# Kernel optimization log

Hardware: AMD Instinct MI355X
Metric: run time of the kernel (lower is better)

Reference implementation:

```python
import jax, jax.numpy as jnp
import numpy as np

D_IN, D_H, BATCH = 4096, 512, 8192


def _layernorm(x, g, b, eps=1e-5):
    mu = jnp.mean(x, axis=-1, keepdims=True)
    var = jnp.var(x, axis=-1, keepdims=True)
    return (x - mu) * jax.lax.rsqrt(var + eps) * g + b


def setup_inputs() -> dict:
    key = jax.random.key(0)
    ks = jax.random.split(key, 10)
    x = jax.random.normal(ks[0], (BATCH, D_IN), jnp.float32)
    h = jax.random.normal(ks[1], (BATCH, D_H), jnp.float32)
    s1 = 1.0 / np.sqrt(D_IN + D_H)
    W1 = jax.random.uniform(ks[2], (D_IN + D_H, D_H), jnp.float32, -s1, s1)
    b1 = jnp.zeros((D_H,), jnp.float32)
    ln1_g = jnp.ones((D_H,), jnp.float32)
    ln1_b = jnp.zeros((D_H,), jnp.float32)
    s2 = 1.0 / np.sqrt(D_H)
    W2 = jax.random.uniform(ks[3], (D_H, 3 * D_H), jnp.float32, -s2, s2)
    b2 = jnp.zeros((3 * D_H,), jnp.float32)
    base_tau = jnp.ones((D_H,), jnp.float32)  # time_constant_init = 1.0
    base_A = jax.random.normal(ks[4], (D_H, D_H), jnp.float32) * 0.1
    idx = jnp.arange(D_H)
    base_A = base_A.at[idx, idx].set(-0.5)
    base_B = jax.random.normal(ks[5], (D_IN, D_H), jnp.float32) * 0.1
    hn_g = jnp.ones((D_H,), jnp.float32)
    hn_b = jnp.zeros((D_H,), jnp.float32)
    return {"x": x, "h": h, "W1": W1, "b1": b1, "ln1_g": ln1_g, "ln1_b": ln1_b,
            "W2": W2, "b2": b2, "base_tau": base_tau, "base_A": base_A,
            "base_B": base_B, "hn_g": hn_g, "hn_b": hn_b}


def reference(x, h, W1, b1, ln1_g, ln1_b, W2, b2, base_tau, base_A, base_B, hn_g, hn_b):
    dt = 0.1
    # time_net hypernetwork
    xh = jnp.concatenate([x, h], axis=-1)                 # [B, D_IN+D_H]
    t = _layernorm(xh @ W1 + b1, ln1_g, ln1_b)
    t = jax.nn.gelu(t, approximate=False)
    params = t @ W2 + b2                                  # [B, 3*D_H]
    tau_s, A_s, B_s = jnp.split(params, 3, axis=-1)
    tau = base_tau * (jax.nn.sigmoid(tau_s) * 2.0)        # [B, D_H]
    A_row = 1.0 + 0.5 * jnp.tanh(A_s)                     # per-sample row scale of A
    B_col = 1.0 + 0.5 * jnp.tanh(B_s)                     # per-sample col scale of B
    # A[b] = base_A * A_row[b][:,None]; h @ A[b].T == (h @ base_A.T) * A_row[b]
    recurrent = (h @ base_A.T) * A_row                    # [B, D_H]
    # B[b] = base_B * B_col[b][None,:]; x @ B[b] == (x @ base_B) * B_col[b]
    input_term = (x @ base_B) * B_col                     # [B, D_H]
    dhdt = -h / (tau + 1e-8) + jnp.tanh(recurrent + input_term)
    new_h = _layernorm(h + dt * dhdt, hn_g, hn_b)
    return new_h
```

## Files before the change

kernel.cpp:

```cpp
#include <hip/hip_runtime.h>

#define BATCH 8192
#define DIN 4096
#define DH 512

typedef float f32x4 __attribute__((ext_vector_type(4)));
typedef float f32x2 __attribute__((ext_vector_type(2)));
typedef short s16x8 __attribute__((ext_vector_type(8)));
typedef unsigned short u16x2 __attribute__((ext_vector_type(2)));
typedef unsigned short u16x4 __attribute__((ext_vector_type(4)));
typedef unsigned short u16x8 __attribute__((ext_vector_type(8)));

static __device__ __forceinline__ unsigned short f2bf(float f) {
  unsigned int u = __float_as_uint(f);
  u += 0x7FFFu + ((u >> 16) & 1u);
  return (unsigned short)(u >> 16);
}
static __device__ __forceinline__ float bf2f(unsigned short s) {
  return __uint_as_float(((unsigned int)s) << 16);
}

typedef const __attribute__((address_space(1))) unsigned int* gas_ptr;
typedef __attribute__((address_space(3))) unsigned int* las_ptr;
static __device__ __forceinline__ void gl_lds16(const unsigned short* g, unsigned short* l) {
  __builtin_amdgcn_global_load_lds((gas_ptr)g, (las_ptr)l, 16, 0, 0);
}

static __device__ __forceinline__ void transpose_body(
    const float* __restrict__ in, int C,
    unsigned short* __restrict__ out, int ldo, int row_off,
    int bx, int by, float (*tl)[33])
{
  const int tid = threadIdx.x;
  const int tx = tid & 31, ty = tid >> 5;
  const int c0 = bx * 32, r0 = by * 32;
#pragma unroll
  for (int i = 0; i < 4; i++)
    tl[ty + 8 * i][tx] = in[(size_t)(r0 + ty + 8 * i) * C + c0 + tx];
  __syncthreads();
#pragma unroll
  for (int i = 0; i < 4; i++)
    out[(size_t)(row_off + c0 + ty + 8 * i) * ldo + r0 + tx] = f2bf(tl[tx][ty + 8 * i]);
}

__global__ __launch_bounds__(256) void prep_all_k(
    const float* __restrict__ x, unsigned short* __restrict__ xbf,
    const float* __restrict__ h, unsigned short* __restrict__ hbf,
    const float* __restrict__ base_A, unsigned short* __restrict__ Abf,
    const float* __restrict__ W1, const float* __restrict__ base_B,
    unsigned short* __restrict__ BTcat,
    const float* __restrict__ W2, unsigned short* __restrict__ W2T)
{
  __shared__ float tl[32][33];
  const int b = blockIdx.x;
  const int tid = threadIdx.x;
  const int KC = DIN + DH;
  if (b < 32768) {
    const int i = (b * 256 + tid) * 4;
    f32x4 v = *(const f32x4*)(x + i);
    u16x4 p = { f2bf(v[0]), f2bf(v[1]), f2bf(v[2]), f2bf(v[3]) };
    *(u16x4*)(xbf + i) = p;
  } else if (b < 36864) {
    const int i = ((b - 32768) * 256 + tid) * 4;
    f32x4 v = *(const f32x4*)(h + i);
    u16x4 p = { f2bf(v[0]), f2bf(v[1]), f2bf(v[2]), f2bf(v[3]) };
    *(u16x4*)(hbf + i) = p;
  } else if (b < 37120) {
    const int i = ((b - 36864) * 256 + tid) * 4;
    f32x4 v = *(const f32x4*)(base_A + i);
    u16x4 p = { f2bf(v[0]), f2bf(v[1]), f2bf(v[2]), f2bf(v[3]) };
    *(u16x4*)(Abf + i) = p;
  } else if (b < 39424) {
    const int bb = b - 37120;
    transpose_body(W1, DH, BTcat, KC, 0, bb & 15, bb >> 4, tl);
  } else if (b < 41472) {
    const int bb = b - 39424;
    transpose_body(base_B, DH, BTcat, KC, DH, bb & 15, bb >> 4, tl);
  } else if (b < 41600) {
    const int gid = (b - 41472) * 256 + tid;
    const int row = gid >> 6, c = (gid & 63) * 8;
    u16x8 z = { 0, 0, 0, 0, 0, 0, 0, 0 };
    *(u16x8*)(BTcat + (size_t)(DH + row) * KC + DIN + c) = z;
  } else {
    const int bb = b - 41600;
    transpose_body(W2, 3 * DH, W2T, DH, 0, bb % 48, bb / 48, tl);
  }
}

template<int EPI>
static __device__ __forceinline__ void gemm2_engine(
    const unsigned short* __restrict__ A0, int lda0, int K0,
    const unsigned short* __restrict__ A1, int lda1,
    const unsigned short* __restrict__ BT, int ldb,
    unsigned short* __restrict__ C0, int ldc,
    unsigned short* __restrict__ C1,
    const float* __restrict__ bias,
    const float* __restrict__ base_tau,
    int mb, int nb, int K, char* smem)
{
  unsigned short* As = (unsigned short*)smem;
  unsigned short* Bs = (unsigned short*)(smem + 32768);
  float* red = (float*)smem;

  const int tid = threadIdx.x;
  const int lane = tid & 63;
  const int wid = tid >> 6;
  const int grp = wid >> 2;
  const int wg  = wid & 3;
  const int wm = (wg >> 1) * 64;
  const int wn = (wg & 1) * 64;
  const int srow = lane >> 2;
  const int scol = ((lane & 3) ^ ((lane >> 3) & 3)) * 8;
  const int fr = lane & 15;
  const int fk = ((lane >> 4) ^ ((lane >> 1) & 3)) * 8;
  const int NT2 = K / 64;

  f32x4 acc[4][4];
#pragma unroll
  for (int i = 0; i < 4; i++)
#pragma unroll
    for (int j = 0; j < 4; j++)
      acc[i][j] = (f32x4){ 0.f, 0.f, 0.f, 0.f };

  auto STAGE = [&](int buf, int per) {
    const int tk = 2 * per + grp;
    const int k0 = tk * 32;
    const bool s0 = (k0 < K0);
    const unsigned short* Ab = s0 ? A0 : A1;
    const int ld = s0 ? lda0 : lda1;
    const int ko = (s0 ? k0 : k0 - K0) + scol;
    unsigned short* ab = As + (grp * 2 + buf) * 4096 + (32 * wg) * 32;
    unsigned short* bb = Bs + (grp * 2 + buf) * 4096 + (32 * wg) * 32;
#pragma unroll
    for (int c = 0; c < 2; c++) {
      const int r = 32 * wg + c * 16 + srow;
      gl_lds16(Ab + (size_t)(mb + r) * ld + ko, ab + c * 16 * 32);
      gl_lds16(BT + (size_t)(nb + r) * ldb + k0 + scol, bb + c * 16 * 32);
    }
  };

  STAGE(0, 0);
  asm volatile("s_waitcnt vmcnt(0)" ::: "memory");
  __builtin_amdgcn_s_barrier();

  int buf = 0;
  for (int t = 0; t < NT2; t++) {
    if (t + 1 < NT2) STAGE(buf ^ 1, t + 1);

    const unsigned short* ar = As + (grp * 2 + buf) * 4096;
    const unsigned short* br = Bs + (grp * 2 + buf) * 4096;
    s16x8 af[4], bv[4];
#pragma unroll
    for (int mi = 0; mi < 4; mi++)
      af[mi] = *(const s16x8*)(ar + (wm + mi * 16 + fr) * 32 + fk);
#pragma unroll
    for (int ni = 0; ni < 4; ni++)
      bv[ni] = *(const s16x8*)(br + (wn + ni * 16 + fr) * 32 + fk);

    asm volatile("s_waitcnt lgkmcnt(0)" ::: "memory");
    __builtin_amdgcn_sched_barrier(0);

#pragma unroll
    for (int mi = 0; mi < 4; mi++)
#pragma unroll
      for (int ni = 0; ni < 4; ni++)
        acc[mi][ni] = __builtin_amdgcn_mfma_f32_16x16x32_bf16(
            af[mi], bv[ni], acc[mi][ni], 0, 0, 0);

    asm volatile("s_waitcnt vmcnt(0)" ::: "memory");
    __builtin_amdgcn_s_barrier();
    buf ^= 1;
  }

  if (grp == 1) {
#pragma unroll
    for (int mi = 0; mi < 4; mi++)
#pragma unroll
      for (int ni = 0; ni < 4; ni++)
        *(f32x4*)(red + (((wg * 4 + mi) * 4 + ni) * 64 + lane) * 4) = acc[mi][ni];
  }
  __syncthreads();
  if (grp != 0) return;

  const int rb = (lane >> 4) * 4;
#pragma unroll
  for (int mi = 0; mi < 4; mi++) {
#pragma unroll
    for (int ni = 0; ni < 4; ni++) {
      f32x4 o = *(const f32x4*)(red + (((wg * 4 + mi) * 4 + ni) * 64 + lane) * 4);
      acc[mi][ni] += o;
#pragma unroll
      for (int r = 0; r < 4; r++) {
        const int row = mb + wm + mi * 16 + rb + r;
        const int col = nb + wn + ni * 16 + fr;
        float v = acc[mi][ni][r];
        if (EPI == 3) {
          if (col < DH) C0[(size_t)row * DH + col] = f2bf(v + bias[col]);
          else          C1[(size_t)row * DH + (col - DH)] = f2bf(v);
        } else if (EPI == 2) {
          C0[(size_t)row * ldc + col] = f2bf(v);
        } else if (EPI == 1) {
          v += bias[col];
          if ((col >> 9) == 0) {
            const float s = 1.0f / (1.0f + expf(-v));
            v = 1.0f / (base_tau[col & (DH - 1)] * 2.0f * s + 1e-8f);
          } else {
            v = 1.0f + 0.5f * tanhf(v);
          }
          C0[(size_t)row * ldc + col] = f2bf(v);
        }
      }
    }
  }
}

__global__ __launch_bounds__(512, 4) void fused_gemm_k(
    const unsigned short* __restrict__ xbf,
    const unsigned short* __restrict__ hbf,
    const unsigned short* __restrict__ BTcat,
    unsigned short* __restrict__ pre1,
    unsigned short* __restrict__ rawB,
    const float* __restrict__ b1)
{
  __shared__ __align__(16) char smem[65536];
  const int cpx = gridDim.x >> 3;
  const int virt = (blockIdx.x & 7) * cpx + (blockIdx.x >> 3);
  const int mb = (virt & 63) * 128;
  const int nb = (virt >> 6) * 128;
  gemm2_engine<3>(xbf, DIN, DIN, hbf, DH, BTcat, DIN + DH,
                  pre1, DH, rawB, b1, nullptr, mb, nb, DIN + DH, smem);
}

__global__ __launch_bounds__(512, 4) void tail_gemm_k(
    const unsigned short* __restrict__ hbf,
    const unsigned short* __restrict__ Abf,
    const unsigned short* __restrict__ tbf,
    const unsigned short* __restrict__ W2T,
    unsigned short* __restrict__ rawA,
    unsigned short* __restrict__ scales,
    const float* __restrict__ b2,
    const float* __restrict__ base_tau)
{
  __shared__ __align__(16) char smem[65536];
  const int b = blockIdx.x;
  if (b < 768) {
    const int mb = (b & 63) * 128, nb = (b >> 6) * 128;
    gemm2_engine<1>(tbf, DH, DH, nullptr, 0, W2T, DH,
                    scales, 3 * DH, nullptr, b2, base_tau, mb, nb, DH, smem);
  } else {
    const int b2i = b - 768;
    const int mb = (b2i & 63) * 128, nb = (b2i >> 6) * 128;
    gemm2_engine<2>(hbf, DH, DH, nullptr, 0, Abf, DH,
                    rawA, DH, nullptr, nullptr, nullptr, mb, nb, DH, smem);
  }
}

__device__ __forceinline__ float block_sum256(float v, float* red) {
#pragma unroll
  for (int m = 32; m >= 1; m >>= 1) v += __shfl_xor(v, m, 64);
  __syncthreads();
  if ((threadIdx.x & 63) == 0) red[threadIdx.x >> 6] = v;
  __syncthreads();
  return red[0] + red[1] + red[2] + red[3];
}

__global__ __launch_bounds__(256) void ln_gelu_k(
    const unsigned short* __restrict__ pre,
    const float* __restrict__ g, const float* __restrict__ b,
    unsigned short* __restrict__ t)
{
  __shared__ float red[4];
  const int row = blockIdx.x;
  const int c = threadIdx.x * 2;
  const size_t ro = (size_t)row * DH;
  u16x2 raw = *(const u16x2*)(pre + ro + c);
  const float v0 = bf2f(raw[0]), v1 = bf2f(raw[1]);
  const float mu = block_sum256(v0 + v1, red) * (1.0f / DH);
  const float d0 = v0 - mu, d1 = v1 - mu;
  const float var = block_sum256(d0 * d0 + d1 * d1, red) * (1.0f / DH);
  const float inv = rsqrtf(var + 1e-5f);
  const float y0 = d0 * inv * g[c] + b[c];
  const float y1 = d1 * inv * g[c + 1] + b[c + 1];
  u16x2 o = { f2bf(0.5f * y0 * (1.0f + erff(y0 * 0.70710678118f))),
              f2bf(0.5f * y1 * (1.0f + erff(y1 * 0.70710678118f))) };
  *(u16x2*)(t + ro + c) = o;
}

__global__ __launch_bounds__(256) void final_k(
    const float* __restrict__ h,
    const unsigned short* __restrict__ rawA,
    const unsigned short* __restrict__ rawB,
    const unsigned short* __restrict__ scales,
    const float* __restrict__ hn_g, const float* __restrict__ hn_b,
    float* __restrict__ out)
{
  __shared__ float red[4];
  const int row = blockIdx.x;
  const int c = threadIdx.x * 2;
  const size_t ro = (size_t)row * DH;
  f32x2 hv = *(const f32x2*)(h + ro + c);
  u16x2 ra = *(const u16x2*)(rawA + ro + c);
  u16x2 rb = *(const u16x2*)(rawB + ro + c);
  const unsigned short* sc = scales + (size_t)row * (3 * DH);
  u16x2 ti  = *(const u16x2*)(sc + c);
  u16x2 arw = *(const u16x2*)(sc + DH + c);
  u16x2 bcl = *(const u16x2*)(sc + 2 * DH + c);
  const float u0 = hv[0] + 0.1f * (-hv[0] * bf2f(ti[0])
                 + tanhf(bf2f(ra[0]) * bf2f(arw[0]) + bf2f(rb[0]) * bf2f(bcl[0])));
  const float u1 = hv[1] + 0.1f * (-hv[1] * bf2f(ti[1])
                 + tanhf(bf2f(ra[1]) * bf2f(arw[1]) + bf2f(rb[1]) * bf2f(bcl[1])));
  const float mu = block_sum256(u0 + u1, red) * (1.0f / DH);
  const float d0 = u0 - mu, d1 = u1 - mu;
  const float var = block_sum256(d0 * d0 + d1 * d1, red) * (1.0f / DH);
  const float inv = rsqrtf(var + 1e-5f);
  f32x2 o = { d0 * inv * hn_g[c] + hn_b[c],
              d1 * inv * hn_g[c + 1] + hn_b[c + 1] };
  *(f32x2*)(out + ro + c) = o;
}

extern "C" void kernel_launch(void* const* d_in, const int* in_sizes, int n_in,
                              void* d_out, int out_size, void* d_ws, size_t ws_size,
                              hipStream_t stream)
{
  const float* x        = (const float*)d_in[0];
  const float* h        = (const float*)d_in[1];
  const float* W1       = (const float*)d_in[2];
  const float* b1       = (const float*)d_in[3];
  const float* ln1_g    = (const float*)d_in[4];
  const float* ln1_b    = (const float*)d_in[5];
  const float* W2       = (const float*)d_in[6];
  const float* b2       = (const float*)d_in[7];
  const float* base_tau = (const float*)d_in[8];
  const float* base_A   = (const float*)d_in[9];
  const float* base_B   = (const float*)d_in[10];
  const float* hn_g     = (const float*)d_in[11];
  const float* hn_b     = (const float*)d_in[12];

  char* w = (char*)d_ws;
  unsigned short* xbf    = (unsigned short*)(w);
  unsigned short* hbf    = (unsigned short*)(w + 67108864);
  unsigned short* BTcat  = (unsigned short*)(w + 75497472);
  unsigned short* tbf    = (unsigned short*)(w + 75497472);
  unsigned short* W2T    = (unsigned short*)(w + 84934656);
  unsigned short* Abf    = (unsigned short*)(w + 86507520);
  unsigned short* pre1   = (unsigned short*)(w + 87031808);
  unsigned short* rawA   = (unsigned short*)(w + 87031808);
  unsigned short* rawB   = (unsigned short*)(w + 95420416);
  unsigned short* scales = (unsigned short*)(w + 103809024);

  prep_all_k<<<42368, 256, 0, stream>>>(x, xbf, h, hbf, base_A, Abf,
                                        W1, base_B, BTcat, W2, W2T);

  fused_gemm_k<<<512, 512, 0, stream>>>(xbf, hbf, BTcat, pre1, rawB, b1);
  ln_gelu_k<<<BATCH, 256, 0, stream>>>(pre1, ln1_g, ln1_b, tbf);
  tail_gemm_k<<<1024, 512, 0, stream>>>(hbf, Abf, tbf, W2T, rawA, scales, b2, base_tau);
  final_k<<<BATCH, 256, 0, stream>>>(h, rawA, rawB, scales, hn_g, hn_b, (float*)d_out);
}
```

Before: 215.8 us.

## Interleave GEMM prefetch and LDS fragment loads with MFMA phases

Splits each K-iteration of the GEMM main loop into four phases, one per B column fragment. Loading of the next B fragment and the global-to-LDS prefetch of the next A and B tiles are spread across these phases. MFMA runs are wrapped in s_setprio to raise wave priority during compute. The aim is to overlap memory issue with matrix math instead of waiting on all LDS reads up front. In exchange there are four barriers per iteration instead of one, and correctness relies on the compiler honouring the implicit waits on LDS reads before each MFMA.

```diff
diff --git a/kernel.cpp b/kernel.cpp
--- a/kernel.cpp
+++ b/kernel.cpp
@@ -122,7 +122,7 @@
     for (int j = 0; j < 4; j++)
       acc[i][j] = (f32x4){ 0.f, 0.f, 0.f, 0.f };
 
-  auto STAGE = [&](int buf, int per) {
+  auto STAGE_A = [&](int buf, int per) {
     const int tk = 2 * per + grp;
     const int k0 = tk * 32;
     const bool s0 = (k0 < K0);
@@ -130,45 +130,58 @@
     const int ld = s0 ? lda0 : lda1;
     const int ko = (s0 ? k0 : k0 - K0) + scol;
     unsigned short* ab = As + (grp * 2 + buf) * 4096 + (32 * wg) * 32;
-    unsigned short* bb = Bs + (grp * 2 + buf) * 4096 + (32 * wg) * 32;
 #pragma unroll
     for (int c = 0; c < 2; c++) {
       const int r = 32 * wg + c * 16 + srow;
       gl_lds16(Ab + (size_t)(mb + r) * ld + ko, ab + c * 16 * 32);
+    }
+  };
+  auto STAGE_B = [&](int buf, int per) {
+    const int tk = 2 * per + grp;
+    const int k0 = tk * 32;
+    unsigned short* bb = Bs + (grp * 2 + buf) * 4096 + (32 * wg) * 32;
+#pragma unroll
+    for (int c = 0; c < 2; c++) {
+      const int r = 32 * wg + c * 16 + srow;
       gl_lds16(BT + (size_t)(nb + r) * ldb + k0 + scol, bb + c * 16 * 32);
     }
   };
 
-  STAGE(0, 0);
+  STAGE_A(0, 0);
+  STAGE_B(0, 0);
   asm volatile("s_waitcnt vmcnt(0)" ::: "memory");
   __builtin_amdgcn_s_barrier();
 
   int buf = 0;
   for (int t = 0; t < NT2; t++) {
-    if (t + 1 < NT2) STAGE(buf ^ 1, t + 1);
-
     const unsigned short* ar = As + (grp * 2 + buf) * 4096;
     const unsigned short* br = Bs + (grp * 2 + buf) * 4096;
     s16x8 af[4], bv[4];
 #pragma unroll
     for (int mi = 0; mi < 4; mi++)
       af[mi] = *(const s16x8*)(ar + (wm + mi * 16 + fr) * 32 + fk);
-#pragma unroll
-    for (int ni = 0; ni < 4; ni++)
-      bv[ni] = *(const s16x8*)(br + (wn + ni * 16 + fr) * 32 + fk);
-
-    asm volatile("s_waitcnt lgkmcnt(0)" ::: "memory");
-    __builtin_amdgcn_sched_barrier(0);
-
-#pragma unroll
-    for (int mi = 0; mi < 4; mi++)
-#pragma unroll
-      for (int ni = 0; ni < 4; ni++)
-        acc[mi][ni] = __builtin_amdgcn_mfma_f32_16x16x32_bf16(
-            af[mi], bv[ni], acc[mi][ni], 0, 0, 0);
-
-    asm volatile("s_waitcnt vmcnt(0)" ::: "memory");
-    __builtin_amdgcn_s_barrier();
+    bv[0] = *(const s16x8*)(br + (wn + fr) * 32 + fk);
+
+#pragma unroll
+    for (int p = 0; p < 4; p++) {
+      if (p < 3)
+        bv[p + 1] = *(const s16x8*)(br + (wn + (p + 1) * 16 + fr) * 32 + fk);
+      if (p == 0 && t + 1 < NT2) STAGE_A(buf ^ 1, t + 1);
+      if (p == 1 && t + 1 < NT2) STAGE_B(buf ^ 1, t + 1);
+
+      __builtin_amdgcn_s_setprio(1);
+#pragma unroll
+      for (int mi = 0; mi < 4; mi++)
+        acc[mi][p] = __builtin_amdgcn_mfma_f32_16x16x32_bf16(
+            af[mi], bv[p], acc[mi][p], 0, 0, 0);
+      __builtin_amdgcn_s_setprio(0);
+
+      if (p == 3) {
+        asm volatile("s_waitcnt vmcnt(0) lgkmcnt(0)" ::: "memory");
+        __builtin_amdgcn_sched_barrier(0);
+      }
+      __builtin_amdgcn_s_barrier();
+    }
     buf ^= 1;
   }
 
```

Result: no change. 213.9 us, median of 3 (-0.9%).
